# Kernel optimization log

Measured on AMD Instinct MI355X. Metric: run time of the kernel, lower is better.

## Reference

```python
import jax, jax.numpy as jnp
import numpy as np
import math

FEATURE_DIM = 64  # head dim; scale = 1/sqrt(FEATURE_DIM)
B, H, S, D = 2, 12, 4096, FEATURE_DIM


def setup_inputs() -> dict:
    key = jax.random.key(0)
    kq, kk, kv = jax.random.split(key, 3)
    return {
        "query": jax.random.normal(kq, (B, H, S, D), dtype=jnp.float32),
        "key": jax.random.normal(kk, (B, H, S, D), dtype=jnp.float32),
        "value": jax.random.normal(kv, (B, H, S, D), dtype=jnp.float32),
    }


def reference(query, key, value):
    scale = 1.0 / math.sqrt(FEATURE_DIM)
    # [B,H,S,S] score matrix, exactly as the naive torch module materializes it
    scores = jnp.einsum("bhqd,bhkd->bhqk", query, key) * scale
    weights = jax.nn.softmax(scores, axis=-1)
    return jnp.einsum("bhqk,bhkd->bhqd", weights, value)
```

## Files before the change

### kernel.cpp

```cpp
#include <hip/hip_runtime.h>


typedef float f32x4 __attribute__((ext_vector_type(4)));
typedef float f32x16 __attribute__((ext_vector_type(16)));
typedef short short8 __attribute__((ext_vector_type(8)));
typedef __bf16 bf16x8 __attribute__((ext_vector_type(8)));
typedef __bf16 bf16x2 __attribute__((ext_vector_type(2)));
typedef unsigned u32x4 __attribute__((ext_vector_type(4)));

#define NB 2
#define NH 12
#define NHEADS (NB * NH)
#define SEQ 4096
#define HD 64
#define QBLK 128
#define KVBLK 64
#define NT (SEQ / KVBLK)
#define NQB (SEQ / QBLK)
#define TILE_BYTES (KVBLK * HD * 2)
#define WS_NEEDED ((size_t)NHEADS * SEQ * HD * 2 * 2)
#define QSCALE 0.1803368801111244f

__device__ __forceinline__ unsigned short f2bf(float x) {
    unsigned u = __builtin_bit_cast(unsigned, x);
    u += 0x7fffu + ((u >> 16) & 1u);
    return (unsigned short)(u >> 16);
}

__device__ __forceinline__ float fexp2(float x) {
#if __has_builtin(__builtin_amdgcn_exp2f)
    return __builtin_amdgcn_exp2f(x);
#else
    float r;
    asm("v_exp_f32 %0, %1" : "=v"(r) : "v"(x));
    return r;
#endif
}

__device__ __forceinline__ int swz(int row, int colByte) {
    return row * 128 + (colByte ^ ((row & 7) << 4));
}

__device__ __forceinline__ unsigned pkbf(float lo, float hi) {
    bf16x2 t;
    t[0] = (__bf16)lo;
    t[1] = (__bf16)hi;
    return __builtin_bit_cast(unsigned, t);
}

__device__ __forceinline__ void plswap(unsigned& a, unsigned& b) {
    asm volatile("v_permlane32_swap_b32 %0, %1" : "+v"(a), "+v"(b));
}

__device__ __forceinline__ void dot2one(float& acc, unsigned p, unsigned ones) {
    asm("v_dot2_f32_bf16 %0, %1, %2, %0" : "+v"(acc) : "v"(p), "v"(ones));
}

__device__ __forceinline__ f32x16 zero16() {
    f32x16 z = {0.f,0.f,0.f,0.f,0.f,0.f,0.f,0.f,0.f,0.f,0.f,0.f,0.f,0.f,0.f,0.f};
    return z;
}

__global__ __launch_bounds__(256) void conv_k(const float* __restrict__ Kg,
                                              char* __restrict__ Kw) {
    const int g = blockIdx.x * 256 + threadIdx.x;
    const int e0 = g * 8;
    const int head = e0 >> 18;
    const int rem = e0 & (262144 - 1);
    const int row = rem >> 6;
    const int col = rem & 63;
    const int tile = row >> 6;
    const int r = row & 63;
    f32x4 a = *(const f32x4*)(Kg + (size_t)e0);
    f32x4 b = *(const f32x4*)(Kg + (size_t)e0 + 4);
    short8 t;
    #pragma unroll
    for (int j = 0; j < 4; ++j) {
        t[j]     = (short)f2bf(a[j]);
        t[j + 4] = (short)f2bf(b[j]);
    }
    *(short8*)(Kw + ((size_t)head * NT + tile) * TILE_BYTES + swz(r, col * 2)) = t;
}

__global__ __launch_bounds__(256) void conv_vt(const float* __restrict__ Vg,
                                               char* __restrict__ Vw) {
    __shared__ float tile[64][65];
    const int b = blockIdx.x;
    const int tid = threadIdx.x;
    const float* src = Vg + (size_t)b * (KVBLK * HD);
    const int r = tid >> 2;
    const int c = (tid & 3) * 16;
    f32x4 v[4];
    #pragma unroll
    for (int j = 0; j < 4; ++j) v[j] = *(const f32x4*)(src + r * 64 + c + j * 4);
    #pragma unroll
    for (int j = 0; j < 16; ++j) tile[r][c + j] = v[j >> 2][j & 3];
    __syncthreads();
    const int f = r;
    const int k0 = c;
    char* dst = Vw + (size_t)b * TILE_BYTES;
    short8 t0, t1;
    #pragma unroll
    for (int j = 0; j < 8; ++j) {
        t0[j] = (short)f2bf(tile[k0 + j][f]);
        t1[j] = (short)f2bf(tile[k0 + 8 + j][f]);
    }
    *(short8*)(dst + swz(f, k0 * 2)) = t0;
    *(short8*)(dst + swz(f, k0 * 2 + 16)) = t1;
}

__global__ __launch_bounds__(256, 3) void attn_v9(
    const float* __restrict__ Qg, const char* __restrict__ Kw,
    const char* __restrict__ Vw, float* __restrict__ Og)
{
    __shared__ short Ksm[2][KVBLK * HD];
    __shared__ short Vsm[2][KVBLK * HD];

    const int tid = threadIdx.x;
    const int w  = tid >> 6;
    const int l  = tid & 63;
    const int lq = l & 31;
    const int b5 = l >> 5;

    const int bid = blockIdx.x;
    const int work = (bid & 7) * (NHEADS * NQB / 8) + (bid >> 3);
    const int head = work / NQB;
    const int qb = work % NQB;
    const size_t hoff = (size_t)head * SEQ * HD;
    const int qrow = qb * QBLK + w * 32 + lq;

    short8 qf[4];
    {
        const float* qp = Qg + hoff + (size_t)qrow * HD + b5 * 8;
        #pragma unroll
        for (int dl = 0; dl < 4; ++dl) {
            f32x4 a = *(const f32x4*)(qp + dl * 16);
            f32x4 b = *(const f32x4*)(qp + dl * 16 + 4);
            short8 t;
            #pragma unroll
            for (int j = 0; j < 4; ++j) {
                t[j]     = (short)f2bf(a[j] * QSCALE);
                t[j + 4] = (short)f2bf(b[j] * QSCALE);
            }
            qf[dl] = t;
        }
    }

    float Lv0 = 0.f, Lv1 = 0.f, Lv2 = 0.f, Lv3 = 0.f;
    f32x16 o0 = zero16(), o1 = zero16();
    const f32x16 ZERO = zero16();
    const unsigned ones2 = 0x3F803F80u;

    const char* const kbase = Kw + (size_t)head * NT * TILE_BYTES;
    const char* const vbase = Vw + (size_t)head * NT * TILE_BYTES;

    const int lbase = lq * 128 ^ ((lq & 7) << 4) ^ (b5 * 16);

    auto stage = [&](int buf, int t) {
        const char* gsrc = ((w < 2) ? kbase : vbase) + (size_t)t * TILE_BYTES
                           + (w & 1) * 4096 + l * 16;
        char* lb = (w < 2) ? ((char*)Ksm[buf] + (w & 1) * 4096)
                           : ((char*)Vsm[buf] + (w & 1) * 4096);
        #pragma unroll
        for (int j = 0; j < 4; ++j) {
            __builtin_amdgcn_global_load_lds(
                (const __attribute__((address_space(1))) void*)(gsrc + j * 1024),
                (__attribute__((address_space(3))) void*)(lb + j * 1024),
                16, 0, 0);
        }
    };

    auto body = [&](const char* Kb, const char* Vb) {
        f32x16 s0, s1;
        __builtin_amdgcn_s_setprio(1);
        {
            short8 ka = *(const short8*)(Kb + (lbase ^ 0));
            short8 kb = *(const short8*)(Kb + (lbase ^ 0) + 4096);
            s0 = __builtin_amdgcn_mfma_f32_32x32x16_bf16(
                __builtin_bit_cast(bf16x8, ka), __builtin_bit_cast(bf16x8, qf[0]), ZERO, 0, 0, 0);
            s1 = __builtin_amdgcn_mfma_f32_32x32x16_bf16(
                __builtin_bit_cast(bf16x8, kb), __builtin_bit_cast(bf16x8, qf[0]), ZERO, 0, 0, 0);
        }
        #pragma unroll
        for (int dl = 1; dl < 4; ++dl) {
            short8 ka = *(const short8*)(Kb + (lbase ^ (dl * 32)));
            short8 kb = *(const short8*)(Kb + (lbase ^ (dl * 32)) + 4096);
            s0 = __builtin_amdgcn_mfma_f32_32x32x16_bf16(
                __builtin_bit_cast(bf16x8, ka), __builtin_bit_cast(bf16x8, qf[dl]), s0, 0, 0, 0);
            s1 = __builtin_amdgcn_mfma_f32_32x32x16_bf16(
                __builtin_bit_cast(bf16x8, kb), __builtin_bit_cast(bf16x8, qf[dl]), s1, 0, 0, 0);
        }
        __builtin_amdgcn_s_setprio(0);

        #pragma unroll
        for (int i = 0; i < 16; ++i) s0[i] = fexp2(s0[i]);
        #pragma unroll
        for (int i = 0; i < 16; ++i) s1[i] = fexp2(s1[i]);

        unsigned pw0[8], pw1[8];
        #pragma unroll
        for (int qd = 0; qd < 4; ++qd) {
            pw0[2 * qd]     = pkbf(s0[qd * 4 + 0], s0[qd * 4 + 1]);
            pw0[2 * qd + 1] = pkbf(s0[qd * 4 + 2], s0[qd * 4 + 3]);
            pw1[2 * qd]     = pkbf(s1[qd * 4 + 0], s1[qd * 4 + 1]);
            pw1[2 * qd + 1] = pkbf(s1[qd * 4 + 2], s1[qd * 4 + 3]);
        }

        dot2one(Lv0, pw0[0], ones2); dot2one(Lv1, pw0[1], ones2);
        dot2one(Lv2, pw0[2], ones2); dot2one(Lv3, pw0[3], ones2);
        dot2one(Lv0, pw0[4], ones2); dot2one(Lv1, pw0[5], ones2);
        dot2one(Lv2, pw0[6], ones2); dot2one(Lv3, pw0[7], ones2);
        dot2one(Lv0, pw1[0], ones2); dot2one(Lv1, pw1[1], ones2);
        dot2one(Lv2, pw1[2], ones2); dot2one(Lv3, pw1[3], ones2);
        dot2one(Lv0, pw1[4], ones2); dot2one(Lv1, pw1[5], ones2);
        dot2one(Lv2, pw1[6], ones2); dot2one(Lv3, pw1[7], ones2);

        u32x4 pf[4];
        {
            unsigned a, b, c, d;
            a = pw0[0]; b = pw0[2]; plswap(a, b);
            c = pw0[1]; d = pw0[3]; plswap(c, d);
            pf[0][0] = a; pf[0][1] = c; pf[0][2] = b; pf[0][3] = d;
            a = pw0[4]; b = pw0[6]; plswap(a, b);
            c = pw0[5]; d = pw0[7]; plswap(c, d);
            pf[1][0] = a; pf[1][1] = c; pf[1][2] = b; pf[1][3] = d;
            a = pw1[0]; b = pw1[2]; plswap(a, b);
            c = pw1[1]; d = pw1[3]; plswap(c, d);
            pf[2][0] = a; pf[2][1] = c; pf[2][2] = b; pf[2][3] = d;
            a = pw1[4]; b = pw1[6]; plswap(a, b);
            c = pw1[5]; d = pw1[7]; plswap(c, d);
            pf[3][0] = a; pf[3][1] = c; pf[3][2] = b; pf[3][3] = d;
        }

        __builtin_amdgcn_s_setprio(1);
        #pragma unroll
        for (int kc = 0; kc < 4; ++kc) {
            short8 va0 = *(const short8*)(Vb + (lbase ^ (kc * 32)));
            short8 va1 = *(const short8*)(Vb + (lbase ^ (kc * 32)) + 4096);
            o0 = __builtin_amdgcn_mfma_f32_32x32x16_bf16(
                __builtin_bit_cast(bf16x8, va0), __builtin_bit_cast(bf16x8, pf[kc]), o0, 0, 0, 0);
            o1 = __builtin_amdgcn_mfma_f32_32x32x16_bf16(
                __builtin_bit_cast(bf16x8, va1), __builtin_bit_cast(bf16x8, pf[kc]), o1, 0, 0, 0);
        }
        __builtin_amdgcn_s_setprio(0);
    };

    stage(0, 0);

    for (int t = 0; t < NT; t += 2) {
        __syncthreads();
        stage(1, t + 1);
        body((const char*)Ksm[0], (const char*)Vsm[0]);
        __syncthreads();
        if (t + 2 < NT) stage(0, t + 2);
        body((const char*)Ksm[1], (const char*)Vsm[1]);
    }

    float L = (Lv0 + Lv1) + (Lv2 + Lv3);
    L += __shfl_xor(L, 32);
    const float inv = 1.0f / L;
    float* op = Og + hoff + (size_t)qrow * HD;
    #pragma unroll
    for (int qd = 0; qd < 4; ++qd) {
        const int d0 = 8 * qd + 4 * b5;
        f32x4 v0, v1;
        #pragma unroll
        for (int e = 0; e < 4; ++e) { v0[e] = o0[qd * 4 + e] * inv; v1[e] = o1[qd * 4 + e] * inv; }
        *(f32x4*)(op + d0) = v0;
        *(f32x4*)(op + 32 + d0) = v1;
    }
}

typedef __bf16 bf16x4 __attribute__((ext_vector_type(4)));

__global__ __launch_bounds__(256, 4) void attn_v1(
    const float* __restrict__ Qg, const float* __restrict__ Kg,
    const float* __restrict__ Vg, float* __restrict__ Og)
{
    __shared__ short Ksm[KVBLK * HD];
    __shared__ short Vsm[HD * KVBLK];
    __shared__ short Psm[4 * 16 * KVBLK];

    const int tid = threadIdx.x;
    const int w  = tid >> 6;
    const int l  = tid & 63;
    const int lg = l >> 4;
    const int ll = l & 15;

    const int head = blockIdx.y;
    const size_t hoff = (size_t)head * SEQ * HD;
    const int qbase = blockIdx.x * 64 + w * 16;

    short8 qf[2];
    {
        const float* qp = Qg + hoff + (size_t)(qbase + ll) * HD + lg * 8;
        #pragma unroll
        for (int c = 0; c < 2; ++c) {
            f32x4 a = *(const f32x4*)(qp + c * 32);
            f32x4 b = *(const f32x4*)(qp + c * 32 + 4);
            short8 t;
            #pragma unroll
            for (int j = 0; j < 4; ++j) {
                t[j]     = (short)f2bf(a[j] * 0.125f);
                t[j + 4] = (short)f2bf(b[j] * 0.125f);
            }
            qf[c] = t;
        }
    }

    float M[4], L[4];
    f32x4 o[4];
    const f32x4 zero = {0.f, 0.f, 0.f, 0.f};
    #pragma unroll
    for (int jj = 0; jj < 4; ++jj) { M[jj] = -1e30f; L[jj] = 0.f; }
    #pragma unroll
    for (int dt = 0; dt < 4; ++dt) o[dt] = zero;

    const int r0 = tid >> 3;
    const int c0 = (tid & 7) * 8;
    char* const Kb = (char*)Ksm;
    char* const Vb = (char*)Vsm;
    char* const Pb = (char*)Psm + w * (16 * KVBLK * 2);

    for (int t = 0; t < NT; ++t) {
        const int kv0 = t * KVBLK;
        __syncthreads();
        #pragma unroll
        for (int half = 0; half < 2; ++half) {
            const int r = r0 + half * 32;
            const float* kp = Kg + hoff + (size_t)(kv0 + r) * HD + c0;
            f32x4 a = *(const f32x4*)kp;
            f32x4 b = *(const f32x4*)(kp + 4);
            short8 kv;
            #pragma unroll
            for (int j = 0; j < 4; ++j) {
                kv[j]     = (short)f2bf(a[j]);
                kv[j + 4] = (short)f2bf(b[j]);
            }
            *(short8*)(Kb + swz(r, c0 * 2)) = kv;

            const float* vp = Vg + hoff + (size_t)(kv0 + r) * HD + c0;
            f32x4 va = *(const f32x4*)vp;
            f32x4 vb2 = *(const f32x4*)(vp + 4);
            #pragma unroll
            for (int j = 0; j < 4; ++j) {
                *(short*)(Vb + swz(c0 + j,     r * 2)) = (short)f2bf(va[j]);
                *(short*)(Vb + swz(c0 + 4 + j, r * 2)) = (short)f2bf(vb2[j]);
            }
        }
        __syncthreads();

        f32x4 sc[4];
        #pragma unroll
        for (int ct = 0; ct < 4; ++ct) {
            f32x4 acc = zero;
            #pragma unroll
            for (int c = 0; c < 2; ++c) {
                short8 kb = *(const short8*)(Kb + swz(ct * 16 + ll, (c * 32 + lg * 8) * 2));
                acc = __builtin_amdgcn_mfma_f32_16x16x32_bf16(
                    __builtin_bit_cast(bf16x8, qf[c]),
                    __builtin_bit_cast(bf16x8, kb), acc, 0, 0, 0);
            }
            sc[ct] = acc;
        }

        #pragma unroll
        for (int jj = 0; jj < 4; ++jj) {
            float m = fmaxf(fmaxf(sc[0][jj], sc[1][jj]), fmaxf(sc[2][jj], sc[3][jj]));
            m = fmaxf(m, __shfl_xor(m, 1));
            m = fmaxf(m, __shfl_xor(m, 2));
            m = fmaxf(m, __shfl_xor(m, 4));
            m = fmaxf(m, __shfl_xor(m, 8));
            const float mn = fmaxf(M[jj], m);
            const float corr = __expf(M[jj] - mn);
            M[jj] = mn;
            float p0 = __expf(sc[0][jj] - mn);
            float p1 = __expf(sc[1][jj] - mn);
            float p2 = __expf(sc[2][jj] - mn);
            float p3 = __expf(sc[3][jj] - mn);
            sc[0][jj] = p0; sc[1][jj] = p1; sc[2][jj] = p2; sc[3][jj] = p3;
            float s = (p0 + p1) + (p2 + p3);
            s += __shfl_xor(s, 1);
            s += __shfl_xor(s, 2);
            s += __shfl_xor(s, 4);
            s += __shfl_xor(s, 8);
            L[jj] = L[jj] * corr + s;
            #pragma unroll
            for (int dt = 0; dt < 4; ++dt) o[dt][jj] *= corr;
        }

        #pragma unroll
        for (int ct = 0; ct < 4; ++ct) {
            #pragma unroll
            for (int jj = 0; jj < 4; ++jj) {
                *(short*)(Pb + swz(lg * 4 + jj, (ct * 16 + ll) * 2)) =
                    (short)f2bf(sc[ct][jj]);
            }
        }

        #pragma unroll
        for (int kc = 0; kc < 2; ++kc) {
            short8 pa = *(const short8*)(Pb + swz(ll, (kc * 32 + lg * 8) * 2));
            #pragma unroll
            for (int dt = 0; dt < 4; ++dt) {
                short8 vbf = *(const short8*)(Vb + swz(dt * 16 + ll, (kc * 32 + lg * 8) * 2));
                o[dt] = __builtin_amdgcn_mfma_f32_16x16x32_bf16(
                    __builtin_bit_cast(bf16x8, pa),
                    __builtin_bit_cast(bf16x8, vbf), o[dt], 0, 0, 0);
            }
        }
    }

    float* op = Og + hoff;
    #pragma unroll
    for (int jj = 0; jj < 4; ++jj) {
        const float inv = 1.0f / L[jj];
        const int q = qbase + lg * 4 + jj;
        #pragma unroll
        for (int dt = 0; dt < 4; ++dt)
            op[(size_t)q * HD + dt * 16 + ll] = o[dt][jj] * inv;
    }
}

extern "C" void kernel_launch(void* const* d_in, const int* in_sizes, int n_in,
                              void* d_out, int out_size, void* d_ws, size_t ws_size,
                              hipStream_t stream) {
    const float* Q = (const float*)d_in[0];
    const float* K = (const float*)d_in[1];
    const float* V = (const float*)d_in[2];
    float* O = (float*)d_out;

    if (ws_size >= WS_NEEDED) {
        char* Kw = (char*)d_ws;
        char* Vw = Kw + (size_t)NHEADS * SEQ * HD * 2;
        conv_k<<<NHEADS * SEQ * HD / (8 * 256), 256, 0, stream>>>(K, Kw);
        conv_vt<<<NHEADS * NT, 256, 0, stream>>>(V, Vw);
        attn_v9<<<NHEADS * NQB, 256, 0, stream>>>(Q, Kw, Vw, O);
    } else {
        dim3 grid(SEQ / 64, NHEADS);
        attn_v1<<<grid, 256, 0, stream>>>(Q, K, V, O);
    }
}
```

Baseline: 130.2 us.

## Load V fragments directly from global in MFMA layout, drop V LDS staging

The V conversion kernel now writes each transposed bf16 tile in a per-lane fragment order that matches the MFMA operand layout. The attention kernel drops the V shared-memory double buffer and has each lane read its eight V fragments straight from global memory (via cache) during the softmax step. This halves LDS use and staging traffic per tile and removes the LDS reads for V, but it exposes global-load latency inside the loop body and adds register pressure from the eight prefetched fragments.

```diff
diff --git a/kernel.cpp b/kernel.cpp
--- a/kernel.cpp
+++ b/kernel.cpp
@@ -98,23 +98,25 @@
     __syncthreads();
     const int f = r;
     const int k0 = c;
-    char* dst = Vw + (size_t)b * TILE_BYTES;
+    const int kc = k0 >> 4;
+    const int h = f >> 5;
+    const int lq = f & 31;
+    char* dst = Vw + (size_t)b * TILE_BYTES + (kc * 2 + h) * 1024;
     short8 t0, t1;
     #pragma unroll
     for (int j = 0; j < 8; ++j) {
         t0[j] = (short)f2bf(tile[k0 + j][f]);
         t1[j] = (short)f2bf(tile[k0 + 8 + j][f]);
     }
-    *(short8*)(dst + swz(f, k0 * 2)) = t0;
-    *(short8*)(dst + swz(f, k0 * 2 + 16)) = t1;
-}
-
-__global__ __launch_bounds__(256, 3) void attn_v9(
+    *(short8*)(dst + lq * 16) = t0;
+    *(short8*)(dst + (lq + 32) * 16) = t1;
+}
+
+__global__ __launch_bounds__(256, 3) void attn_v10(
     const float* __restrict__ Qg, const char* __restrict__ Kw,
     const char* __restrict__ Vw, float* __restrict__ Og)
 {
     __shared__ short Ksm[2][KVBLK * HD];
-    __shared__ short Vsm[2][KVBLK * HD];
 
     const int tid = threadIdx.x;
     const int w  = tid >> 6;
@@ -152,17 +154,15 @@
     const unsigned ones2 = 0x3F803F80u;
 
     const char* const kbase = Kw + (size_t)head * NT * TILE_BYTES;
-    const char* const vbase = Vw + (size_t)head * NT * TILE_BYTES;
+    const char* const vlane = Vw + (size_t)head * NT * TILE_BYTES + l * 16;
 
     const int lbase = lq * 128 ^ ((lq & 7) << 4) ^ (b5 * 16);
 
-    auto stage = [&](int buf, int t) {
-        const char* gsrc = ((w < 2) ? kbase : vbase) + (size_t)t * TILE_BYTES
-                           + (w & 1) * 4096 + l * 16;
-        char* lb = (w < 2) ? ((char*)Ksm[buf] + (w & 1) * 4096)
-                           : ((char*)Vsm[buf] + (w & 1) * 4096);
-        #pragma unroll
-        for (int j = 0; j < 4; ++j) {
+    auto stageK = [&](int buf, int t) {
+        const char* gsrc = kbase + (size_t)t * TILE_BYTES + w * 2048 + l * 16;
+        char* lb = (char*)Ksm[buf] + w * 2048;
+        #pragma unroll
+        for (int j = 0; j < 2; ++j) {
             __builtin_amdgcn_global_load_lds(
                 (const __attribute__((address_space(1))) void*)(gsrc + j * 1024),
                 (__attribute__((address_space(3))) void*)(lb + j * 1024),
@@ -170,7 +170,7 @@
         }
     };
 
-    auto body = [&](const char* Kb, const char* Vb) {
+    auto body = [&](const char* Kb, const char* vt) {
         f32x16 s0, s1;
         __builtin_amdgcn_s_setprio(1);
         {
@@ -191,6 +191,11 @@
                 __builtin_bit_cast(bf16x8, kb), __builtin_bit_cast(bf16x8, qf[dl]), s1, 0, 0, 0);
         }
         __builtin_amdgcn_s_setprio(0);
+
+        short8 vf[8];
+        #pragma unroll
+        for (int c = 0; c < 8; ++c)
+            vf[c] = *(const short8*)(vt + c * 1024);
 
         #pragma unroll
         for (int i = 0; i < 16; ++i) s0[i] = fexp2(s0[i]);
@@ -235,25 +240,25 @@
         __builtin_amdgcn_s_setprio(1);
         #pragma unroll
         for (int kc = 0; kc < 4; ++kc) {
-            short8 va0 = *(const short8*)(Vb + (lbase ^ (kc * 32)));
-            short8 va1 = *(const short8*)(Vb + (lbase ^ (kc * 32)) + 4096);
             o0 = __builtin_amdgcn_mfma_f32_32x32x16_bf16(
-                __builtin_bit_cast(bf16x8, va0), __builtin_bit_cast(bf16x8, pf[kc]), o0, 0, 0, 0);
+                __builtin_bit_cast(bf16x8, vf[kc * 2 + 0]),
+                __builtin_bit_cast(bf16x8, pf[kc]), o0, 0, 0, 0);
             o1 = __builtin_amdgcn_mfma_f32_32x32x16_bf16(
-                __builtin_bit_cast(bf16x8, va1), __builtin_bit_cast(bf16x8, pf[kc]), o1, 0, 0, 0);
+                __builtin_bit_cast(bf16x8, vf[kc * 2 + 1]),
+                __builtin_bit_cast(bf16x8, pf[kc]), o1, 0, 0, 0);
         }
         __builtin_amdgcn_s_setprio(0);
     };
 
-    stage(0, 0);
+    stageK(0, 0);
 
     for (int t = 0; t < NT; t += 2) {
         __syncthreads();
-        stage(1, t + 1);
-        body((const char*)Ksm[0], (const char*)Vsm[0]);
+        stageK(1, t + 1);
+        body((const char*)Ksm[0], vlane + (size_t)t * TILE_BYTES);
         __syncthreads();
-        if (t + 2 < NT) stage(0, t + 2);
-        body((const char*)Ksm[1], (const char*)Vsm[1]);
+        if (t + 2 < NT) stageK(0, t + 2);
+        body((const char*)Ksm[1], vlane + (size_t)(t + 1) * TILE_BYTES);
     }
 
     float L = (Lv0 + Lv1) + (Lv2 + Lv3);
@@ -435,7 +440,7 @@
         char* Vw = Kw + (size_t)NHEADS * SEQ * HD * 2;
         conv_k<<<NHEADS * SEQ * HD / (8 * 256), 256, 0, stream>>>(K, Kw);
         conv_vt<<<NHEADS * NT, 256, 0, stream>>>(V, Vw);
-        attn_v9<<<NHEADS * NQB, 256, 0, stream>>>(Q, Kw, Vw, O);
+        attn_v10<<<NHEADS * NQB, 256, 0, stream>>>(Q, Kw, Vw, O);
     } else {
         dim3 grid(SEQ / 64, NHEADS);
         attn_v1<<<grid, 256, 0, stream>>>(Q, K, V, O);
```

Measured after the change: 134.7 us. 3.5% more time.
